# Optimization experiments

Hardware: AMD Instinct MI355X
Metric: run time of the kernel (lower is better)

Reference implementation:

```python
import jax, jax.numpy as jnp
import numpy as np

KERNEL_SIZE = 5


def setup_inputs() -> dict:
    key = jax.random.key(0)
    k1, k2, k3 = jax.random.split(key, 3)
    B, H, W = 32, 512, 512
    f = jax.random.uniform(k1, (B, H, W), dtype=jnp.float32)          # distribution function, non-negative
    K = jax.random.normal(k2, (KERNEL_SIZE, KERNEL_SIZE, H, W), dtype=jnp.float32) * 0.01  # per-pixel kernels
    dt = jax.random.uniform(k3, (B,), dtype=jnp.float32) * 0.1        # per-batch timestep
    return {"f": f, "K": K, "dt": dt}


def reference(f, K, dt):
    # f: (B,H,W); K: (k,k,H,W) position-dependent (unshared) kernels; dt: (B,)
    # Equivalent to: patches = unfold(pad(f)); df = einsum('bkv,kv->bv', patches, K.reshape(k*k,-1))
    # Implemented as a sum over the k*k kernel taps of shifted slices (avoids the
    # B*k^2*H*W patches tensor; loop is over the fixed kernel footprint, not data dims).
    k = K.shape[0]
    B, H, W = f.shape
    pl, pr = k // 2, (k - 1) // 2  # matches pad_size = (k//2, (k-1)//2)*2
    f_pad = jnp.pad(f, ((0, 0), (pl, pr), (pl, pr)))  # 'zeros' padding_mode
    df = jnp.zeros_like(f)
    for i in range(k):
        for j in range(k):
            df = df + f_pad[:, i:i + H, j:j + W] * K[i, j]
    out = f + df * dt[:, None, None]
    return jnp.maximum(out, 0.0)  # ensure_non_negative_f clamp
```

## Files before the change

### kernel.cpp

```cpp
#include <hip/hip_runtime.h>

#define H 512
#define W 512
#define BATCH 32
#define KS 5
#define B_CHUNK 4
#define LROW 520
#define LTILE (6 * LROW)
#define LDS_FLOATS (B_CHUNK * LTILE)

typedef const __attribute__((address_space(1))) void gv_t;
typedef __attribute__((address_space(3))) void lv_t;
typedef float nf4 __attribute__((ext_vector_type(4)));

__device__ __forceinline__ void async_cp16(const float* src, float* lds_dst) {
    __builtin_amdgcn_global_load_lds((gv_t*)src, (lv_t*)lds_dst, 16, 0, 0);
}

__global__ __launch_bounds__(256, 3) void op2d_kernel(
    const float* __restrict__ f,
    const float* __restrict__ K,
    const float* __restrict__ dt,
    float* __restrict__ out)
{
    __shared__ float lds[LDS_FLOATS];

    const int tid   = threadIdx.x;
    const int lane  = tid & 63;
    const int wave  = tid >> 6;
    const int w0    = (tid & 127) * 4;
    const int lr    = tid >> 7;
    const int h0    = blockIdx.x * 2;
    const int chunk = blockIdx.y;
    const int h     = h0 + lr;

#pragma unroll
    for (int idx = tid; idx < LDS_FLOATS; idx += 256) lds[idx] = 0.f;
    __syncthreads();

    {
        const int b  = wave;
        const int bg = chunk * B_CHUNK + b;
        const float* fb = f + (size_t)bg * H * W;
#pragma unroll
        for (int k = 0; k < 12; ++k) {
            const int r    = k >> 1;
            const int half = k & 1;
            const int gr   = h0 - 2 + r;
            if (gr >= 0 && gr < H) {
                const float* src = fb + (size_t)gr * W + half * 256 + lane * 4;
                float* dst = lds + b * LTILE + r * LROW + 4 + half * 256;
                async_cp16(src, dst);
            }
        }
    }

    const float* Kbase = K + (size_t)h * W + w0;
    float4 Kv[2][KS];
#pragma unroll
    for (int j = 0; j < KS; ++j)
        Kv[0][j] = *reinterpret_cast<const float4*>(Kbase + (size_t)j * (H * W));

    __syncthreads();

    float acc[B_CHUNK][4];
#pragma unroll
    for (int b = 0; b < B_CHUNK; ++b)
#pragma unroll
        for (int p = 0; p < 4; ++p) acc[b][p] = 0.f;

    float fc[B_CHUNK][4];

#pragma unroll
    for (int i = 0; i < KS; ++i) {
        if (i + 1 < KS) {
#pragma unroll
            for (int j = 0; j < KS; ++j)
                Kv[(i + 1) & 1][j] = *reinterpret_cast<const float4*>(
                    Kbase + (size_t)((i + 1) * KS + j) * (H * W));
        }
        const float4* Kc = Kv[i & 1];

#pragma unroll
        for (int b = 0; b < B_CHUNK; ++b) {
            const float* row = lds + b * LTILE + (lr + i) * LROW + w0;
            const float4 ra = *reinterpret_cast<const float4*>(row);
            const float4 rb = *reinterpret_cast<const float4*>(row + 4);
            const float4 rc = *reinterpret_cast<const float4*>(row + 8);
            const float buf[12] = { ra.x, ra.y, ra.z, ra.w,
                                    rb.x, rb.y, rb.z, rb.w,
                                    rc.x, rc.y, rc.z, rc.w };
            if (i == 2) { fc[b][0] = rb.x; fc[b][1] = rb.y;
                          fc[b][2] = rb.z; fc[b][3] = rb.w; }
#pragma unroll
            for (int j = 0; j < KS; ++j) {
                acc[b][0] += Kc[j].x * buf[j + 2];
                acc[b][1] += Kc[j].y * buf[j + 3];
                acc[b][2] += Kc[j].z * buf[j + 4];
                acc[b][3] += Kc[j].w * buf[j + 5];
            }
        }
    }

#pragma unroll
    for (int b = 0; b < B_CHUNK; ++b) {
        const int bg = chunk * B_CHUNK + b;
        const float dtb = dt[bg];
        nf4 o;
        o.x = fmaxf(fc[b][0] + acc[b][0] * dtb, 0.f);
        o.y = fmaxf(fc[b][1] + acc[b][1] * dtb, 0.f);
        o.z = fmaxf(fc[b][2] + acc[b][2] * dtb, 0.f);
        o.w = fmaxf(fc[b][3] + acc[b][3] * dtb, 0.f);
        __builtin_nontemporal_store(o,
            reinterpret_cast<nf4*>(out + ((size_t)bg * H + h) * W + w0));
    }
}

extern "C" void kernel_launch(void* const* d_in, const int* in_sizes, int n_in,
                              void* d_out, int out_size, void* d_ws, size_t ws_size,
                              hipStream_t stream) {
    const float* f  = (const float*)d_in[0];
    const float* K  = (const float*)d_in[1];
    const float* dt = (const float*)d_in[2];
    float* out = (float*)d_out;

    dim3 block(256);
    dim3 grid(H / 2, BATCH / B_CHUNK);
    op2d_kernel<<<grid, block, 0, stream>>>(f, K, dt, out);
}
```

Before: 120.7 us.

## Stream rows through an LDS ring buffer across multiple row steps per block

Each block now handles 8 output rows over 4 steps with 2 batches, keeping an 8-row circular LDS buffer per batch. Only the 2 new halo rows are prefetched asynchronously for the next step while the current one computes. This cuts the redundant halo reloads of f from 3x to about 1.5x per row and overlaps those loads with compute. In exchange, each block reuses K across only 2 batches instead of 4, so K traffic roughly doubles, and a barrier is added per step.

```diff
diff --git a/kernel.cpp b/kernel.cpp
--- a/kernel.cpp
+++ b/kernel.cpp
@@ -2,12 +2,15 @@
 
 #define H 512
 #define W 512
+#define HW (H * W)
 #define BATCH 32
 #define KS 5
-#define B_CHUNK 4
+#define B_CHUNK 2
+#define RING 8
 #define LROW 520
-#define LTILE (6 * LROW)
+#define LTILE (RING * LROW)
 #define LDS_FLOATS (B_CHUNK * LTILE)
+#define STEPS 4
 
 typedef const __attribute__((address_space(1))) void gv_t;
 typedef __attribute__((address_space(3))) void lv_t;
@@ -17,7 +20,18 @@
     __builtin_amdgcn_global_load_lds((gv_t*)src, (lv_t*)lds_dst, 16, 0, 0);
 }
 
-__global__ __launch_bounds__(256, 3) void op2d_kernel(
+__device__ __forceinline__ void stage_unit(const float* __restrict__ fb,
+                                           float* ldsb, int gr, int half,
+                                           int lane) {
+    float* dst = ldsb + (gr & 7) * LROW + 4 + half * 256;
+    if (gr >= 0 && gr < H) {
+        async_cp16(fb + (size_t)gr * W + half * 256 + lane * 4, dst);
+    } else {
+        *reinterpret_cast<nf4*>(dst + lane * 4) = (nf4)0.f;
+    }
+}
+
+__global__ __launch_bounds__(256, 4) void op2d_kernel(
     const float* __restrict__ f,
     const float* __restrict__ K,
     const float* __restrict__ dt,
@@ -30,89 +44,110 @@
     const int wave  = tid >> 6;
     const int w0    = (tid & 127) * 4;
     const int lr    = tid >> 7;
-    const int h0    = blockIdx.x * 2;
+    const int hblk  = blockIdx.x * (2 * STEPS);
     const int chunk = blockIdx.y;
-    const int h     = h0 + lr;
+    const int bg0   = chunk * B_CHUNK;
+
+    for (int idx = tid * 4; idx < LDS_FLOATS; idx += 1024)
+        *reinterpret_cast<nf4*>(lds + idx) = (nf4)0.f;
+    __syncthreads();
+
+    const float* fb0 = f + (size_t)bg0 * HW;
+    const float* fb1 = fb0 + HW;
 
 #pragma unroll
-    for (int idx = tid; idx < LDS_FLOATS; idx += 256) lds[idx] = 0.f;
-    __syncthreads();
-
-    {
-        const int b  = wave;
-        const int bg = chunk * B_CHUNK + b;
-        const float* fb = f + (size_t)bg * H * W;
-#pragma unroll
-        for (int k = 0; k < 12; ++k) {
-            const int r    = k >> 1;
-            const int half = k & 1;
-            const int gr   = h0 - 2 + r;
-            if (gr >= 0 && gr < H) {
-                const float* src = fb + (size_t)gr * W + half * 256 + lane * 4;
-                float* dst = lds + b * LTILE + r * LROW + 4 + half * 256;
-                async_cp16(src, dst);
-            }
-        }
+    for (int k = 0; k < 6; ++k) {
+        const int u    = wave * 6 + k;
+        const int bu   = u / 12;
+        const int rem  = u % 12;
+        const int r    = rem >> 1;
+        const int half = rem & 1;
+        stage_unit(bu ? fb1 : fb0, lds + bu * LTILE, hblk - 2 + r, half, lane);
     }
 
-    const float* Kbase = K + (size_t)h * W + w0;
     float4 Kv[2][KS];
+    {
+        const float* Kb = K + (size_t)(hblk + lr) * W + w0;
 #pragma unroll
-    for (int j = 0; j < KS; ++j)
-        Kv[0][j] = *reinterpret_cast<const float4*>(Kbase + (size_t)j * (H * W));
+        for (int j = 0; j < KS; ++j)
+            Kv[0][j] = *reinterpret_cast<const float4*>(Kb + (size_t)j * HW);
+    }
+
+    const float dtb[B_CHUNK] = { dt[bg0], dt[bg0 + 1] };
 
     __syncthreads();
 
-    float acc[B_CHUNK][4];
 #pragma unroll
-    for (int b = 0; b < B_CHUNK; ++b)
+    for (int s = 0; s < STEPS; ++s) {
+        const int hs = hblk + 2 * s;
+        const int h  = hs + lr;
+
+        if (s + 1 < STEPS) {
 #pragma unroll
-        for (int p = 0; p < 4; ++p) acc[b][p] = 0.f;
+            for (int k = 0; k < 2; ++k) {
+                const int u    = wave * 2 + k;
+                const int bu   = u >> 2;
+                const int r    = (u >> 1) & 1;
+                const int half = u & 1;
+                stage_unit(bu ? fb1 : fb0, lds + bu * LTILE, hs + 4 + r, half, lane);
+            }
+        }
 
-    float fc[B_CHUNK][4];
+        const float* Kstep = K + (size_t)h * W + w0;
+        float acc[B_CHUNK][4] = {{0.f, 0.f, 0.f, 0.f}, {0.f, 0.f, 0.f, 0.f}};
+        float fc[B_CHUNK][4];
 
 #pragma unroll
-    for (int i = 0; i < KS; ++i) {
-        if (i + 1 < KS) {
+        for (int i = 0; i < KS; ++i) {
+            const int g = s * KS + i;
+            if (i + 1 < KS) {
 #pragma unroll
-            for (int j = 0; j < KS; ++j)
-                Kv[(i + 1) & 1][j] = *reinterpret_cast<const float4*>(
-                    Kbase + (size_t)((i + 1) * KS + j) * (H * W));
+                for (int j = 0; j < KS; ++j)
+                    Kv[(g + 1) & 1][j] = *reinterpret_cast<const float4*>(
+                        Kstep + (size_t)((i + 1) * KS + j) * HW);
+            } else if (s + 1 < STEPS) {
+                const float* Knext = Kstep + 2 * W;
+#pragma unroll
+                for (int j = 0; j < KS; ++j)
+                    Kv[(g + 1) & 1][j] = *reinterpret_cast<const float4*>(
+                        Knext + (size_t)j * HW);
+            }
+            const float4* Kc = Kv[g & 1];
+
+#pragma unroll
+            for (int b = 0; b < B_CHUNK; ++b) {
+                const int slot = (h + i - 2) & 7;
+                const float* row = lds + b * LTILE + slot * LROW + w0;
+                const float4 ra = *reinterpret_cast<const float4*>(row);
+                const float4 rb = *reinterpret_cast<const float4*>(row + 4);
+                const float4 rc = *reinterpret_cast<const float4*>(row + 8);
+                const float buf[12] = { ra.x, ra.y, ra.z, ra.w,
+                                        rb.x, rb.y, rb.z, rb.w,
+                                        rc.x, rc.y, rc.z, rc.w };
+                if (i == 2) { fc[b][0] = rb.x; fc[b][1] = rb.y;
+                              fc[b][2] = rb.z; fc[b][3] = rb.w; }
+#pragma unroll
+                for (int j = 0; j < KS; ++j) {
+                    acc[b][0] += Kc[j].x * buf[j + 2];
+                    acc[b][1] += Kc[j].y * buf[j + 3];
+                    acc[b][2] += Kc[j].z * buf[j + 4];
+                    acc[b][3] += Kc[j].w * buf[j + 5];
+                }
+            }
         }
-        const float4* Kc = Kv[i & 1];
 
 #pragma unroll
         for (int b = 0; b < B_CHUNK; ++b) {
-            const float* row = lds + b * LTILE + (lr + i) * LROW + w0;
-            const float4 ra = *reinterpret_cast<const float4*>(row);
-            const float4 rb = *reinterpret_cast<const float4*>(row + 4);
-            const float4 rc = *reinterpret_cast<const float4*>(row + 8);
-            const float buf[12] = { ra.x, ra.y, ra.z, ra.w,
-                                    rb.x, rb.y, rb.z, rb.w,
-                                    rc.x, rc.y, rc.z, rc.w };
-            if (i == 2) { fc[b][0] = rb.x; fc[b][1] = rb.y;
-                          fc[b][2] = rb.z; fc[b][3] = rb.w; }
-#pragma unroll
-            for (int j = 0; j < KS; ++j) {
-                acc[b][0] += Kc[j].x * buf[j + 2];
-                acc[b][1] += Kc[j].y * buf[j + 3];
-                acc[b][2] += Kc[j].z * buf[j + 4];
-                acc[b][3] += Kc[j].w * buf[j + 5];
-            }
+            nf4 o;
+            o.x = fmaxf(fc[b][0] + acc[b][0] * dtb[b], 0.f);
+            o.y = fmaxf(fc[b][1] + acc[b][1] * dtb[b], 0.f);
+            o.z = fmaxf(fc[b][2] + acc[b][2] * dtb[b], 0.f);
+            o.w = fmaxf(fc[b][3] + acc[b][3] * dtb[b], 0.f);
+            __builtin_nontemporal_store(o,
+                reinterpret_cast<nf4*>(out + ((size_t)(bg0 + b) * H + h) * W + w0));
         }
-    }
 
-#pragma unroll
-    for (int b = 0; b < B_CHUNK; ++b) {
-        const int bg = chunk * B_CHUNK + b;
-        const float dtb = dt[bg];
-        nf4 o;
-        o.x = fmaxf(fc[b][0] + acc[b][0] * dtb, 0.f);
-        o.y = fmaxf(fc[b][1] + acc[b][1] * dtb, 0.f);
-        o.z = fmaxf(fc[b][2] + acc[b][2] * dtb, 0.f);
-        o.w = fmaxf(fc[b][3] + acc[b][3] * dtb, 0.f);
-        __builtin_nontemporal_store(o,
-            reinterpret_cast<nf4*>(out + ((size_t)bg * H + h) * W + w0));
+        __syncthreads();
     }
 }
 
@@ -125,6 +160,6 @@
     float* out = (float*)d_out;
 
     dim3 block(256);
-    dim3 grid(H / 2, BATCH / B_CHUNK);
+    dim3 grid(H / (2 * STEPS), BATCH / B_CHUNK);
     op2d_kernel<<<grid, block, 0, stream>>>(f, K, dt, out);
 }
```

New measurement: 144.1 us. 1.19x slower.

## Replace LDS tiling with register sliding window over rows per thread

Applied to the files above, without the earlier changes.

Drops the LDS staging and async global-to-LDS copies. Each thread now keeps a 5-row register window of f for 2 batches and marches down 8 output rows, loading one new row per step. Neighbouring columns are read directly from global memory, so overlapping loads rely on cache. The change removes the LDS zero-fill and barriers and reuses vertical rows across output rows, but K reuse per load falls from 4 batches to 2. K traffic therefore doubles, and register pressure rises from the large unrolled window.

```diff
diff --git a/kernel.cpp b/kernel.cpp
--- a/kernel.cpp
+++ b/kernel.cpp
@@ -2,117 +2,124 @@
 
 #define H 512
 #define W 512
+#define HW (H * W)
 #define BATCH 32
 #define KS 5
-#define B_CHUNK 4
-#define LROW 520
-#define LTILE (6 * LROW)
-#define LDS_FLOATS (B_CHUNK * LTILE)
+#define NROWS 8
+#define NB 2
 
-typedef const __attribute__((address_space(1))) void gv_t;
-typedef __attribute__((address_space(3))) void lv_t;
 typedef float nf4 __attribute__((ext_vector_type(4)));
 
-__device__ __forceinline__ void async_cp16(const float* src, float* lds_dst) {
-    __builtin_amdgcn_global_load_lds((gv_t*)src, (lv_t*)lds_dst, 16, 0, 0);
+__device__ __forceinline__ void load_row(const float* __restrict__ fb, int gr,
+                                         bool wl, bool wr, int w0, nf4* d) {
+    if (gr >= 0 && gr < H) {
+        const float* row = fb + (size_t)gr * W;
+        d[0] = wl ? *reinterpret_cast<const nf4*>(row + w0 - 4) : (nf4)0.f;
+        d[1] =      *reinterpret_cast<const nf4*>(row + w0);
+        d[2] = wr ? *reinterpret_cast<const nf4*>(row + w0 + 4) : (nf4)0.f;
+    } else {
+        d[0] = (nf4)0.f; d[1] = (nf4)0.f; d[2] = (nf4)0.f;
+    }
 }
 
-__global__ __launch_bounds__(256, 3) void op2d_kernel(
+__global__ __launch_bounds__(128, 2) void op2d_kernel(
     const float* __restrict__ f,
     const float* __restrict__ K,
     const float* __restrict__ dt,
     float* __restrict__ out)
 {
-    __shared__ float lds[LDS_FLOATS];
+    const int tid  = threadIdx.x;
+    const int w0   = tid * 4;
+    const int hblk = blockIdx.x * NROWS;
+    const int b0   = blockIdx.y * NB;
 
-    const int tid   = threadIdx.x;
-    const int lane  = tid & 63;
-    const int wave  = tid >> 6;
-    const int w0    = (tid & 127) * 4;
-    const int lr    = tid >> 7;
-    const int h0    = blockIdx.x * 2;
-    const int chunk = blockIdx.y;
-    const int h     = h0 + lr;
+    const bool wl = (w0 >= 4);
+    const bool wr = (w0 <= 504);
+
+    const float* fb[NB] = { f + (size_t)b0 * HW, f + (size_t)(b0 + 1) * HW };
+    const float dtb[NB] = { dt[b0], dt[b0 + 1] };
+
+    nf4 win[NB][5][3];
 
 #pragma unroll
-    for (int idx = tid; idx < LDS_FLOATS; idx += 256) lds[idx] = 0.f;
-    __syncthreads();
+    for (int rr = 0; rr < 5; ++rr) {
+#pragma unroll
+        for (int b = 0; b < NB; ++b)
+            load_row(fb[b], hblk - 2 + rr, wl, wr, w0, win[b][rr]);
+    }
 
-    {
-        const int b  = wave;
-        const int bg = chunk * B_CHUNK + b;
-        const float* fb = f + (size_t)bg * H * W;
+    nf4 Kv[2][KS];
 #pragma unroll
-        for (int k = 0; k < 12; ++k) {
-            const int r    = k >> 1;
-            const int half = k & 1;
-            const int gr   = h0 - 2 + r;
-            if (gr >= 0 && gr < H) {
-                const float* src = fb + (size_t)gr * W + half * 256 + lane * 4;
-                float* dst = lds + b * LTILE + r * LROW + 4 + half * 256;
-                async_cp16(src, dst);
+    for (int j = 0; j < KS; ++j)
+        Kv[0][j] = *reinterpret_cast<const nf4*>(
+            K + ((size_t)j * H + hblk) * W + w0);
+
+#pragma unroll
+    for (int s = 0; s < NROWS; ++s) {
+        const int r = hblk + s;
+
+        nf4 nxt[NB][3];
+#pragma unroll
+        for (int b = 0; b < NB; ++b)
+            load_row(fb[b], r + 3, wl, wr, w0, nxt[b]);
+
+        float acc[NB][4] = {{0.f,0.f,0.f,0.f},{0.f,0.f,0.f,0.f}};
+        float fc[NB][4];
+
+#pragma unroll
+        for (int i = 0; i < KS; ++i) {
+            const int g = s * KS + i;
+            if (i + 1 < KS) {
+#pragma unroll
+                for (int j = 0; j < KS; ++j)
+                    Kv[(g + 1) & 1][j] = *reinterpret_cast<const nf4*>(
+                        K + ((size_t)((i + 1) * KS + j) * H + r) * W + w0);
+            } else if (s + 1 < NROWS) {
+#pragma unroll
+                for (int j = 0; j < KS; ++j)
+                    Kv[(g + 1) & 1][j] = *reinterpret_cast<const nf4*>(
+                        K + ((size_t)j * H + (r + 1)) * W + w0);
+            }
+            const nf4* Kc = Kv[g & 1];
+
+#pragma unroll
+            for (int b = 0; b < NB; ++b) {
+                const int slot = (s + i) % 5;
+                const nf4 ra = win[b][slot][0];
+                const nf4 rb = win[b][slot][1];
+                const nf4 rc = win[b][slot][2];
+                const float buf[12] = { ra.x, ra.y, ra.z, ra.w,
+                                        rb.x, rb.y, rb.z, rb.w,
+                                        rc.x, rc.y, rc.z, rc.w };
+                if (i == 2) { fc[b][0] = rb.x; fc[b][1] = rb.y;
+                              fc[b][2] = rb.z; fc[b][3] = rb.w; }
+#pragma unroll
+                for (int j = 0; j < KS; ++j) {
+                    acc[b][0] += Kc[j].x * buf[j + 2];
+                    acc[b][1] += Kc[j].y * buf[j + 3];
+                    acc[b][2] += Kc[j].z * buf[j + 4];
+                    acc[b][3] += Kc[j].w * buf[j + 5];
+                }
             }
         }
-    }
-
-    const float* Kbase = K + (size_t)h * W + w0;
-    float4 Kv[2][KS];
-#pragma unroll
-    for (int j = 0; j < KS; ++j)
-        Kv[0][j] = *reinterpret_cast<const float4*>(Kbase + (size_t)j * (H * W));
-
-    __syncthreads();
-
-    float acc[B_CHUNK][4];
-#pragma unroll
-    for (int b = 0; b < B_CHUNK; ++b)
-#pragma unroll
-        for (int p = 0; p < 4; ++p) acc[b][p] = 0.f;
-
-    float fc[B_CHUNK][4];
 
 #pragma unroll
-    for (int i = 0; i < KS; ++i) {
-        if (i + 1 < KS) {
-#pragma unroll
-            for (int j = 0; j < KS; ++j)
-                Kv[(i + 1) & 1][j] = *reinterpret_cast<const float4*>(
-                    Kbase + (size_t)((i + 1) * KS + j) * (H * W));
+        for (int b = 0; b < NB; ++b) {
+            nf4 o;
+            o.x = fmaxf(fc[b][0] + acc[b][0] * dtb[b], 0.f);
+            o.y = fmaxf(fc[b][1] + acc[b][1] * dtb[b], 0.f);
+            o.z = fmaxf(fc[b][2] + acc[b][2] * dtb[b], 0.f);
+            o.w = fmaxf(fc[b][3] + acc[b][3] * dtb[b], 0.f);
+            __builtin_nontemporal_store(o,
+                reinterpret_cast<nf4*>(out + ((size_t)(b0 + b) * H + r) * W + w0));
         }
-        const float4* Kc = Kv[i & 1];
 
 #pragma unroll
-        for (int b = 0; b < B_CHUNK; ++b) {
-            const float* row = lds + b * LTILE + (lr + i) * LROW + w0;
-            const float4 ra = *reinterpret_cast<const float4*>(row);
-            const float4 rb = *reinterpret_cast<const float4*>(row + 4);
-            const float4 rc = *reinterpret_cast<const float4*>(row + 8);
-            const float buf[12] = { ra.x, ra.y, ra.z, ra.w,
-                                    rb.x, rb.y, rb.z, rb.w,
-                                    rc.x, rc.y, rc.z, rc.w };
-            if (i == 2) { fc[b][0] = rb.x; fc[b][1] = rb.y;
-                          fc[b][2] = rb.z; fc[b][3] = rb.w; }
-#pragma unroll
-            for (int j = 0; j < KS; ++j) {
-                acc[b][0] += Kc[j].x * buf[j + 2];
-                acc[b][1] += Kc[j].y * buf[j + 3];
-                acc[b][2] += Kc[j].z * buf[j + 4];
-                acc[b][3] += Kc[j].w * buf[j + 5];
-            }
+        for (int b = 0; b < NB; ++b) {
+            win[b][s % 5][0] = nxt[b][0];
+            win[b][s % 5][1] = nxt[b][1];
+            win[b][s % 5][2] = nxt[b][2];
         }
-    }
-
-#pragma unroll
-    for (int b = 0; b < B_CHUNK; ++b) {
-        const int bg = chunk * B_CHUNK + b;
-        const float dtb = dt[bg];
-        nf4 o;
-        o.x = fmaxf(fc[b][0] + acc[b][0] * dtb, 0.f);
-        o.y = fmaxf(fc[b][1] + acc[b][1] * dtb, 0.f);
-        o.z = fmaxf(fc[b][2] + acc[b][2] * dtb, 0.f);
-        o.w = fmaxf(fc[b][3] + acc[b][3] * dtb, 0.f);
-        __builtin_nontemporal_store(o,
-            reinterpret_cast<nf4*>(out + ((size_t)bg * H + h) * W + w0));
     }
 }
 
@@ -124,7 +131,7 @@
     const float* dt = (const float*)d_in[2];
     float* out = (float*)d_out;
 
-    dim3 block(256);
-    dim3 grid(H / 2, BATCH / B_CHUNK);
+    dim3 block(128);
+    dim3 grid(H / NROWS, BATCH / NB);
     op2d_kernel<<<grid, block, 0, stream>>>(f, K, dt, out);
 }
```

After: 120.5 us. Within noise of the previous version (-0.2%).
